# Kernel optimization log

Hardware: AMD Instinct MI355X
Metric: run time of the kernel (lower is better)

The kernel has to match this reference:

```python
import jax, jax.numpy as jnp
import numpy as np

N_NODES = 150000
D = 64
N_EDGES = 2000000  # bidirectional: 2 * num_train_edges


def setup_inputs() -> dict:
    key = jax.random.key(0)
    k1, k2, k3, k4, k5 = jax.random.split(key, 5)
    nodes_emb = jax.random.normal(k1, (N_NODES, D), dtype=jnp.float32)
    src = jax.random.randint(k2, (N_EDGES,), 0, N_NODES, dtype=jnp.int64 if jax.config.jax_enable_x64 else jnp.int32).astype(jnp.int32)
    dst = jax.random.randint(k3, (N_EDGES,), 0, N_NODES, dtype=jnp.int32)
    W1 = jax.random.normal(k4, (2 * D, D), dtype=jnp.float32) * (1.0 / np.sqrt(2 * D))
    b1 = jnp.zeros((D,), dtype=jnp.float32)
    W2 = jax.random.normal(k5, (D, 1), dtype=jnp.float32) * (1.0 / np.sqrt(D))
    b2 = jnp.zeros((1,), dtype=jnp.float32)
    return {"nodes_emb": nodes_emb, "src": src, "dst": dst,
            "W1": W1, "b1": b1, "W2": W2, "b2": b2}


def reference(nodes_emb, src, dst, W1, b1, W2, b2):
    # Gather per-edge endpoint embeddings and concat: [E, 2D]
    emb_src = nodes_emb[src]          # [E, D]
    emb_dst = nodes_emb[dst]          # [E, D]
    edge_emb = jnp.concatenate([emb_src, emb_dst], axis=1)  # [E, 2D]
    # 2-layer MLP edge scorer: Linear(2D->D) -> ReLU -> Linear(D->1)
    h = jax.nn.relu(edge_emb @ W1 + b1)  # [E, D]
    edge_logits = h @ W2 + b2            # [E, 1]
    return edge_logits
```

## Files before the change

### kernel.cpp

```cpp
#include <hip/hip_runtime.h>

typedef __attribute__((ext_vector_type(8))) short bf16x8;
typedef __attribute__((ext_vector_type(4))) float f32x4;
typedef __attribute__((ext_vector_type(2))) unsigned int u32x2;
typedef __attribute__((ext_vector_type(4))) unsigned int u32x4;

#define LDSTR 136
#define TPW 8

static __device__ __forceinline__ unsigned int pack2bf(float x, float y) {
  unsigned int ux = __builtin_bit_cast(unsigned int, x);
  ux += 0x7fffu + ((ux >> 16) & 1u);
  unsigned int uy = __builtin_bit_cast(unsigned int, y);
  uy += 0x7fffu + ((uy >> 16) & 1u);
  return (ux >> 16) | (uy & 0xffff0000u);
}
static __device__ __forceinline__ unsigned short f2bf_s(float x) {
  unsigned int ux = __builtin_bit_cast(unsigned int, x);
  ux += 0x7fffu + ((ux >> 16) & 1u);
  return (unsigned short)(ux >> 16);
}
static __device__ __forceinline__ bf16x8 make_afrag(float4 lo, float4 hi) {
  u32x4 p;
  p[0] = pack2bf(lo.x, lo.y);
  p[1] = pack2bf(lo.z, lo.w);
  p[2] = pack2bf(hi.x, hi.y);
  p[3] = pack2bf(hi.z, hi.w);
  return __builtin_bit_cast(bf16x8, p);
}

static __device__ __forceinline__ unsigned int q8(float v, float inv) {
  return (unsigned int)((int)rintf(v * inv) + 128);
}

__global__ __launch_bounds__(256) void node_proj(
    const float* __restrict__ emb,
    const float* __restrict__ W1,
    const float* __restrict__ b1,
    unsigned int* __restrict__ P8,
    unsigned int* __restrict__ Q8,
    float* __restrict__ SP,
    float* __restrict__ SQ,
    int N, int ntiles)
{
  __shared__ unsigned short ls_w1t[64 * LDSTR];
  const int tid  = threadIdx.x;
  const int wave = tid >> 6;
  const int lane = tid & 63;
  const int l15  = lane & 15;
  const int quad = lane >> 4;

  for (int i = tid; i < 64 * 128; i += 256) {
    int k = i >> 6, n = i & 63;
    ls_w1t[n * LDSTR + k] = f2bf_s(W1[i]);
  }
  __syncthreads();

  float b1q[4];
  #pragma unroll
  for (int tn = 0; tn < 4; ++tn) b1q[tn] = b1[tn * 16 + l15];

  bf16x8 bfragP[4][2], bfragQ[4][2];
  #pragma unroll
  for (int tn = 0; tn < 4; ++tn)
    #pragma unroll
    for (int s = 0; s < 2; ++s) {
      bfragP[tn][s] = *(const bf16x8*)&ls_w1t[(tn * 16 + l15) * LDSTR + s * 32 + quad * 8];
      bfragQ[tn][s] = *(const bf16x8*)&ls_w1t[(tn * 16 + l15) * LDSTR + 64 + s * 32 + quad * 8];
    }

  for (int tile = blockIdx.x * 4 + wave; tile < ntiles; tile += gridDim.x * 4) {
    const int base = tile * 16;

    bf16x8 afr0, afr1;
    {
      int node = base + l15;
      node = (node < N) ? node : N - 1;
      const float* rp = emb + (long long)node * 64 + quad * 8;
      afr0 = make_afrag(*(const float4*)(rp),      *(const float4*)(rp + 4));
      afr1 = make_afrag(*(const float4*)(rp + 32), *(const float4*)(rp + 36));
    }

    f32x4 aP[4], aQ[4];
    #pragma unroll
    for (int tn = 0; tn < 4; ++tn) { aP[tn] = (f32x4){0,0,0,0}; aQ[tn] = (f32x4){0,0,0,0}; }
    #pragma unroll
    for (int tn = 0; tn < 4; ++tn) {
      aP[tn] = __builtin_amdgcn_mfma_f32_16x16x32_bf16(afr0, bfragP[tn][0], aP[tn], 0, 0, 0);
      aQ[tn] = __builtin_amdgcn_mfma_f32_16x16x32_bf16(afr0, bfragQ[tn][0], aQ[tn], 0, 0, 0);
      aP[tn] = __builtin_amdgcn_mfma_f32_16x16x32_bf16(afr1, bfragP[tn][1], aP[tn], 0, 0, 0);
      aQ[tn] = __builtin_amdgcn_mfma_f32_16x16x32_bf16(afr1, bfragQ[tn][1], aQ[tn], 0, 0, 0);
    }

    #pragma unroll
    for (int r = 0; r < 4; ++r) {
      const int m = base + quad * 4 + r;
      float vp0 = aP[0][r], vp1 = aP[1][r], vp2 = aP[2][r], vp3 = aP[3][r];
      float vq0 = aQ[0][r] + b1q[0], vq1 = aQ[1][r] + b1q[1];
      float vq2 = aQ[2][r] + b1q[2], vq3 = aQ[3][r] + b1q[3];

      float mp = fmaxf(fmaxf(fabsf(vp0), fabsf(vp1)), fmaxf(fabsf(vp2), fabsf(vp3)));
      float mq = fmaxf(fmaxf(fabsf(vq0), fabsf(vq1)), fmaxf(fabsf(vq2), fabsf(vq3)));
      mp = fmaxf(mp, __shfl_xor(mp, 1)); mq = fmaxf(mq, __shfl_xor(mq, 1));
      mp = fmaxf(mp, __shfl_xor(mp, 2)); mq = fmaxf(mq, __shfl_xor(mq, 2));
      mp = fmaxf(mp, __shfl_xor(mp, 4)); mq = fmaxf(mq, __shfl_xor(mq, 4));
      mp = fmaxf(mp, __shfl_xor(mp, 8)); mq = fmaxf(mq, __shfl_xor(mq, 8));

      const float invP = (mp > 0.f) ? 127.f / mp : 0.f;
      const float invQ = (mq > 0.f) ? 127.f / mq : 0.f;

      if (m < N) {
        unsigned int pw = q8(vp0, invP) | (q8(vp1, invP) << 8) |
                          (q8(vp2, invP) << 16) | (q8(vp3, invP) << 24);
        unsigned int qw = q8(vq0, invQ) | (q8(vq1, invQ) << 8) |
                          (q8(vq2, invQ) << 16) | (q8(vq3, invQ) << 24);
        P8[(long long)m * 16 + l15] = pw;
        Q8[(long long)m * 16 + l15] = qw;
        if (l15 == 0) {
          SP[m] = mp * (1.f / 127.f);
          SQ[m] = mq * (1.f / 127.f);
        }
      }
    }
  }
}

__global__ __launch_bounds__(256) void edge_score(
    const unsigned int* __restrict__ P8,
    const unsigned int* __restrict__ Q8,
    const float* __restrict__ SP,
    const float* __restrict__ SQ,
    const int*   __restrict__ src,
    const int*   __restrict__ dst,
    const float* __restrict__ W2,
    const float* __restrict__ b2,
    float*       __restrict__ out,
    int E)
{
  const int tid  = blockIdx.x * 256 + threadIdx.x;
  const int lane = threadIdx.x & 63;
  const int s    = lane & 7;
  const int g    = lane >> 3;
  const int wid  = tid >> 6;
  const int step = gridDim.x * 4 * 32;

  float w2v[8];
  #pragma unroll
  for (int j = 0; j < 8; ++j) {
    const int pos = s * 8 + j;
    const int ch  = (pos & 3) * 16 + (pos >> 2);
    w2v[j] = W2[ch];
  }
  const float b2v = b2[0];
  const int sd = s * 2;

#define DOT8I(PU, QU, SPv, SQv, ACC)                                          \
  {                                                                           \
    const float t_ = __builtin_fmaf(-128.f, SPv + SQv, 0.f);                  \
    _Pragma("unroll")                                                         \
    for (int k = 0; k < 2; ++k) {                                             \
      const unsigned int pd = PU[k], qd = QU[k];                              \
      _Pragma("unroll")                                                       \
      for (int b = 0; b < 4; ++b) {                                           \
        float pf = (float)((pd >> (8 * b)) & 0xffu);                          \
        float qf = (float)((qd >> (8 * b)) & 0xffu);                          \
        float h = __builtin_fmaf(pf, SPv, __builtin_fmaf(qf, SQv, t_));       \
        h = fmaxf(h, 0.f);                                                    \
        ACC = __builtin_fmaf(h, w2v[k * 4 + b], ACC);                         \
      }                                                                       \
    }                                                                         \
  }

  int e0 = wid * 32;
  if (e0 >= E) return;

  int iA, iB, iC, iD, jA, jB, jC, jD;
  {
    const int eA = e0 + g,      eAc = (eA < E) ? eA : E - 1;
    const int eB = e0 + 8 + g,  eBc = (eB < E) ? eB : E - 1;
    const int eC = e0 + 16 + g, eCc = (eC < E) ? eC : E - 1;
    const int eD = e0 + 24 + g, eDc = (eD < E) ? eD : E - 1;
    iA = src[eAc]; jA = dst[eAc];
    iB = src[eBc]; jB = dst[eBc];
    iC = src[eCc]; jC = dst[eCc];
    iD = src[eDc]; jD = dst[eDc];
  }
  float spA = SP[iA], sqA = SQ[jA];
  float spB = SP[iB], sqB = SQ[jB];
  float spC = SP[iC], sqC = SQ[jC];
  float spD = SP[iD], sqD = SQ[jD];

  while (true) {
    const u32x2 pA = *(const u32x2*)(P8 + iA * 16 + sd);
    const u32x2 qA = *(const u32x2*)(Q8 + jA * 16 + sd);
    const u32x2 pB = *(const u32x2*)(P8 + iB * 16 + sd);
    const u32x2 qB = *(const u32x2*)(Q8 + jB * 16 + sd);
    const u32x2 pC = *(const u32x2*)(P8 + iC * 16 + sd);
    const u32x2 qC = *(const u32x2*)(Q8 + jC * 16 + sd);
    const u32x2 pD = *(const u32x2*)(P8 + iD * 16 + sd);
    const u32x2 qD = *(const u32x2*)(Q8 + jD * 16 + sd);

    const int en = e0 + step;
    const bool more = (en < E);
    int nA = iA, nB = iB, nC = iC, nD = iD;
    int mA = jA, mB = jB, mC = jC, mD = jD;
    if (more) {
      const int fA = en + g,      fAc = (fA < E) ? fA : E - 1;
      const int fB = en + 8 + g,  fBc = (fB < E) ? fB : E - 1;
      const int fC = en + 16 + g, fCc = (fC < E) ? fC : E - 1;
      const int fD = en + 24 + g, fDc = (fD < E) ? fD : E - 1;
      nA = src[fAc]; mA = dst[fAc];
      nB = src[fBc]; mB = dst[fBc];
      nC = src[fCc]; mC = dst[fCc];
      nD = src[fDc]; mD = dst[fDc];
    }

    float accA = 0.f, accB = 0.f, accC = 0.f, accD = 0.f;
    DOT8I(pA, qA, spA, sqA, accA);
    DOT8I(pB, qB, spB, sqB, accB);
    DOT8I(pC, qC, spC, sqC, accC);
    DOT8I(pD, qD, spD, sqD, accD);

    accA += __shfl_xor(accA, 1); accB += __shfl_xor(accB, 1);
    accC += __shfl_xor(accC, 1); accD += __shfl_xor(accD, 1);
    accA += __shfl_xor(accA, 2); accB += __shfl_xor(accB, 2);
    accC += __shfl_xor(accC, 2); accD += __shfl_xor(accD, 2);
    accA += __shfl_xor(accA, 4); accB += __shfl_xor(accB, 4);
    accC += __shfl_xor(accC, 4); accD += __shfl_xor(accD, 4);

    if (s == 0) {
      const int eA = e0 + g;
      const int eB = e0 + 8 + g;
      const int eC = e0 + 16 + g;
      const int eD = e0 + 24 + g;
      if (eA < E) out[eA] = accA + b2v;
      if (eB < E) out[eB] = accB + b2v;
      if (eC < E) out[eC] = accC + b2v;
      if (eD < E) out[eD] = accD + b2v;
    }

    if (!more) break;
    iA = nA; iB = nB; iC = nC; iD = nD;
    jA = mA; jB = mB; jC = mC; jD = mD;
    spA = SP[iA]; sqA = SQ[jA];
    spB = SP[iB]; sqB = SQ[jB];
    spC = SP[iC]; sqC = SQ[jC];
    spD = SP[iD]; sqD = SQ[jD];
    e0 = en;
  }
#undef DOT8I
}

__global__ __launch_bounds__(256) void edge_mlp_f32(
    const float* __restrict__ nodes_emb, const int* __restrict__ src,
    const int* __restrict__ dst, const float* __restrict__ W1,
    const float* __restrict__ b1, const float* __restrict__ W2,
    const float* __restrict__ b2, float* __restrict__ out, int E)
{
  __shared__ unsigned short ls_w1t[64 * LDSTR];
  __shared__ float ls_b1[64];
  __shared__ float ls_w2[64];
  const int tid = threadIdx.x, wave = tid >> 6, lane = tid & 63;
  const int l15 = lane & 15, quad = lane >> 4;
  for (int i = tid; i < 64 * 128; i += 256) {
    int n = i >> 7, k = i & 127;
    ls_w1t[n * LDSTR + k] = f2bf_s(W1[k * 64 + n]);
  }
  if (tid < 64) { ls_b1[tid] = b1[tid]; ls_w2[tid] = W2[tid]; }
  __syncthreads();
  bf16x8 bfrag[4][4];
  #pragma unroll
  for (int tn = 0; tn < 4; ++tn)
    #pragma unroll
    for (int s = 0; s < 4; ++s)
      bfrag[tn][s] = *(const bf16x8*)&ls_w1t[(tn * 16 + l15) * LDSTR + s * 32 + quad * 8];
  float myb1[4], myw2[4];
  #pragma unroll
  for (int tn = 0; tn < 4; ++tn) { myb1[tn] = ls_b1[tn*16+l15]; myw2[tn] = ls_w2[tn*16+l15]; }
  const float b2v = b2[0];
  const int wave_base = blockIdx.x * (TPW * 64) + wave * (TPW * 16);
  #pragma unroll 1
  for (int t = 0; t < TPW; ++t) {
    const int tile_base = wave_base + t * 16;
    if (tile_base >= E) break;
    const int e = tile_base + l15;
    const int si = src[e], di = dst[e];
    const float* srow = nodes_emb + (long long)si * 64 + quad * 8;
    const float* drow = nodes_emb + (long long)di * 64 + quad * 8;
    float4 v0 = *(const float4*)(srow),      v1 = *(const float4*)(srow + 4);
    float4 v2 = *(const float4*)(srow + 32), v3 = *(const float4*)(srow + 36);
    float4 v4 = *(const float4*)(drow),      v5 = *(const float4*)(drow + 4);
    float4 v6 = *(const float4*)(drow + 32), v7 = *(const float4*)(drow + 36);
    bf16x8 afr[4] = {make_afrag(v0,v1), make_afrag(v2,v3), make_afrag(v4,v5), make_afrag(v6,v7)};
    f32x4 acc[4];
    #pragma unroll
    for (int tn = 0; tn < 4; ++tn) acc[tn] = (f32x4){0.f,0.f,0.f,0.f};
    #pragma unroll
    for (int s = 0; s < 4; ++s)
      #pragma unroll
      for (int tn = 0; tn < 4; ++tn)
        acc[tn] = __builtin_amdgcn_mfma_f32_16x16x32_bf16(afr[s], bfrag[tn][s], acc[tn], 0, 0, 0);
    #pragma unroll
    for (int r = 0; r < 4; ++r) {
      float p = 0.f;
      #pragma unroll
      for (int tn = 0; tn < 4; ++tn) {
        float h = fmaxf(acc[tn][r] + myb1[tn], 0.f);
        p = __builtin_fmaf(h, myw2[tn], p);
      }
      p += __shfl_xor(p, 1); p += __shfl_xor(p, 2);
      p += __shfl_xor(p, 4); p += __shfl_xor(p, 8);
      if (l15 == 0) out[tile_base + quad * 4 + r] = p + b2v;
    }
  }
}

extern "C" void kernel_launch(void* const* d_in, const int* in_sizes, int n_in,
                              void* d_out, int out_size, void* d_ws, size_t ws_size,
                              hipStream_t stream) {
  const float* nodes_emb = (const float*)d_in[0];
  const int*   src       = (const int*)d_in[1];
  const int*   dst       = (const int*)d_in[2];
  const float* W1        = (const float*)d_in[3];
  const float* b1        = (const float*)d_in[4];
  const float* W2        = (const float*)d_in[5];
  const float* b2        = (const float*)d_in[6];
  float* out = (float*)d_out;

  const int E = in_sizes[1];
  const int nodes_elems = in_sizes[0];
  const int N = nodes_elems / 64;
  const size_t szRow = (size_t)N * 64;
  const size_t need  = szRow * 2 + (size_t)N * 8;

  if (ws_size >= need) {
    unsigned int* P8 = (unsigned int*)d_ws;
    unsigned int* Q8 = (unsigned int*)((char*)d_ws + szRow);
    float* SP = (float*)((char*)d_ws + szRow * 2);
    float* SQ = (float*)((char*)d_ws + szRow * 2 + (size_t)N * 4);
    const int ntiles = (N + 15) / 16;
    hipLaunchKernelGGL(node_proj, dim3(512), dim3(256), 0, stream,
                       nodes_emb, W1, b1, P8, Q8, SP, SQ, N, ntiles);
    hipLaunchKernelGGL(edge_score, dim3(4096), dim3(256), 0, stream,
                       P8, Q8, SP, SQ, src, dst, W2, b2, out, E);
  } else {
    const int epb = TPW * 64;
    const int blocks = (E + epb - 1) / epb;
    hipLaunchKernelGGL(edge_mlp_f32, dim3(blocks), dim3(256), 0, stream,
                       nodes_emb, src, dst, W1, b1, W2, b2, out, E);
  }
}
```

Measured before the change: 175.9 us.

## Bucketize edges by source/destination node range for cache-local gathers

A new kernel partitions the edges into 64 buckets keyed by (src range, dst range), using LDS atomics per replica block. A second new kernel scores the edges bucket by bucket, locating each edge through a prefix sum and binary search over the per-replica counts. The aim is to keep the quantized P8/Q8 node rows touched by one bucket small enough to stay cache-resident during the random gathers. In exchange it adds a bucketing pass that writes 64-bit packed records to workspace, runs on only 128 blocks, and silently drops edges if a cell exceeds its statistical capacity.

```diff
diff --git a/kernel.cpp b/kernel.cpp
--- a/kernel.cpp
+++ b/kernel.cpp
@@ -1,12 +1,16 @@
 #include <hip/hip_runtime.h>
+#include <math.h>
 
 typedef __attribute__((ext_vector_type(8))) short bf16x8;
 typedef __attribute__((ext_vector_type(4))) float f32x4;
 typedef __attribute__((ext_vector_type(2))) unsigned int u32x2;
 typedef __attribute__((ext_vector_type(4))) unsigned int u32x4;
+typedef unsigned long long u64;
 
 #define LDSTR 136
 #define TPW 8
+#define NREP 128
+#define NBKT 64
 
 static __device__ __forceinline__ unsigned int pack2bf(float x, float y) {
   unsigned int ux = __builtin_bit_cast(unsigned int, x);
@@ -31,6 +35,25 @@
 
 static __device__ __forceinline__ unsigned int q8(float v, float inv) {
   return (unsigned int)((int)rintf(v * inv) + 128);
+}
+
+static __device__ __forceinline__ float dot8i(u32x2 P, u32x2 Q, float sp, float sq,
+                                              const float* w2v) {
+  const float t_ = -128.f * (sp + sq);
+  float acc = 0.f;
+  #pragma unroll
+  for (int k2 = 0; k2 < 2; ++k2) {
+    const unsigned int pd = P[k2], qd = Q[k2];
+    #pragma unroll
+    for (int b = 0; b < 4; ++b) {
+      float pf = (float)((pd >> (8 * b)) & 0xffu);
+      float qf = (float)((qd >> (8 * b)) & 0xffu);
+      float h = __builtin_fmaf(pf, sp, __builtin_fmaf(qf, sq, t_));
+      h = fmaxf(h, 0.f);
+      acc = __builtin_fmaf(h, w2v[k2 * 4 + b], acc);
+    }
+  }
+  return acc;
 }
 
 __global__ __launch_bounds__(256) void node_proj(
@@ -125,17 +148,133 @@
   }
 }
 
+__global__ __launch_bounds__(256) void bucketize(
+    const int* __restrict__ src, const int* __restrict__ dst,
+    u64* __restrict__ seg, unsigned int* __restrict__ cntT,
+    int E, int ndiv, int cap)
+{
+  __shared__ unsigned int curs[NBKT];
+  const int r = blockIdx.x;
+  const int per = (E + NREP - 1) / NREP;
+  const int lo = r * per;
+  const int hi = (lo + per < E) ? lo + per : E;
+  for (int i = threadIdx.x; i < NBKT; i += 256) curs[i] = 0;
+  __syncthreads();
+  for (int e = lo + threadIdx.x; e < hi; e += 256) {
+    const int s = src[e], d = dst[e];
+    const int bkt = (s / ndiv) * 8 + (d / ndiv);
+    const unsigned int pos = atomicAdd(&curs[bkt], 1u);
+    if ((int)pos < cap) {
+      const u64 v = (u64)(unsigned)s | ((u64)(unsigned)d << 18) | ((u64)(unsigned)e << 36);
+      seg[((long long)r * NBKT + bkt) * cap + pos] = v;
+    }
+  }
+  __syncthreads();
+  for (int bkt = threadIdx.x; bkt < NBKT; bkt += 256) {
+    unsigned int c = curs[bkt];
+    cntT[bkt * NREP + r] = (c < (unsigned)cap) ? c : (unsigned)cap;
+  }
+}
+
+__global__ __launch_bounds__(256) void edge_score_bkt(
+    const unsigned int* __restrict__ P8, const unsigned int* __restrict__ Q8,
+    const float* __restrict__ SP, const float* __restrict__ SQ,
+    const u64* __restrict__ seg, const unsigned int* __restrict__ cntT,
+    const float* __restrict__ W2, const float* __restrict__ b2,
+    float* __restrict__ out, int E, int cap)
+{
+  __shared__ unsigned int pref[NREP + 1];
+  const int tid  = threadIdx.x;
+  const int lane = tid & 63;
+  const int sv   = lane & 7;
+  const int g    = lane >> 3;
+  const int wavloc = tid >> 6;
+  const int k    = blockIdx.x & 7;
+  const int tblk = blockIdx.x >> 3;
+  const int ngrp = gridDim.x >> 3;
+  const int wgid = tblk * 4 + wavloc;
+  const int nwg  = ngrp * 4;
+
+  float w2v[8];
+  #pragma unroll
+  for (int j = 0; j < 8; ++j) {
+    const int pos = sv * 8 + j;
+    const int ch  = (pos & 3) * 16 + (pos >> 2);
+    w2v[j] = W2[ch];
+  }
+  const float b2v = b2[0];
+  const int sd = sv * 2;
+
+  #pragma unroll 1
+  for (int j = 0; j < 8; ++j) {
+    const int b = k * 8 + j;
+    __syncthreads();
+    if (tid < 64) {
+      unsigned int c0 = cntT[b * NREP + tid];
+      unsigned int c1 = cntT[b * NREP + 64 + tid];
+      unsigned int s0 = c0, s1 = c1;
+      #pragma unroll
+      for (int off = 1; off < 64; off <<= 1) {
+        unsigned int t0 = __shfl_up(s0, off);
+        unsigned int t1 = __shfl_up(s1, off);
+        if (lane >= off) { s0 += t0; s1 += t1; }
+      }
+      const unsigned int tot0 = __shfl(s0, 63);
+      pref[tid + 1] = s0;
+      pref[64 + tid + 1] = s1 + tot0;
+      if (tid == 0) pref[0] = 0;
+    }
+    __syncthreads();
+    const int T = (int)pref[NREP];
+
+    for (int mb = wgid * 16; mb < T; mb += nwg * 16) {
+      const int mA = mb + g;
+      const int mB = mb + 8 + g;
+      const int mAc = (mA < T) ? mA : T - 1;
+      const int mBc = (mB < T) ? mB : T - 1;
+
+      int rA = 0, rAh = NREP, rB = 0, rBh = NREP;
+      #pragma unroll
+      for (int it = 0; it < 7; ++it) {
+        const int midA = (rA + rAh) >> 1;
+        if ((int)pref[midA] <= mAc) rA = midA; else rAh = midA;
+        const int midB = (rB + rBh) >> 1;
+        if ((int)pref[midB] <= mBc) rB = midB; else rBh = midB;
+      }
+      const u64 vA = seg[((long long)rA * NBKT + b) * cap + (mAc - (int)pref[rA])];
+      const u64 vB = seg[((long long)rB * NBKT + b) * cap + (mBc - (int)pref[rB])];
+      const int sA = (int)(vA & 0x3FFFFu), dA = (int)((vA >> 18) & 0x3FFFFu);
+      const int sB = (int)(vB & 0x3FFFFu), dB = (int)((vB >> 18) & 0x3FFFFu);
+      const int eA = (int)(vA >> 36),      eB = (int)(vB >> 36);
+
+      const u32x2 pA = *(const u32x2*)(P8 + sA * 16 + sd);
+      const u32x2 qA = *(const u32x2*)(Q8 + dA * 16 + sd);
+      const u32x2 pB = *(const u32x2*)(P8 + sB * 16 + sd);
+      const u32x2 qB = *(const u32x2*)(Q8 + dB * 16 + sd);
+      const float spA = SP[sA], sqA = SQ[dA];
+      const float spB = SP[sB], sqB = SQ[dB];
+
+      float accA = dot8i(pA, qA, spA, sqA, w2v);
+      float accB = dot8i(pB, qB, spB, sqB, w2v);
+
+      accA += __shfl_xor(accA, 1); accB += __shfl_xor(accB, 1);
+      accA += __shfl_xor(accA, 2); accB += __shfl_xor(accB, 2);
+      accA += __shfl_xor(accA, 4); accB += __shfl_xor(accB, 4);
+
+      if (sv == 0) {
+        if (mA < T) out[eA] = accA + b2v;
+        if (mB < T) out[eB] = accB + b2v;
+      }
+    }
+  }
+}
+
 __global__ __launch_bounds__(256) void edge_score(
-    const unsigned int* __restrict__ P8,
-    const unsigned int* __restrict__ Q8,
-    const float* __restrict__ SP,
-    const float* __restrict__ SQ,
-    const int*   __restrict__ src,
-    const int*   __restrict__ dst,
-    const float* __restrict__ W2,
-    const float* __restrict__ b2,
-    float*       __restrict__ out,
-    int E)
+    const unsigned int* __restrict__ P8, const unsigned int* __restrict__ Q8,
+    const float* __restrict__ SP, const float* __restrict__ SQ,
+    const int* __restrict__ src, const int* __restrict__ dst,
+    const float* __restrict__ W2, const float* __restrict__ b2,
+    float* __restrict__ out, int E)
 {
   const int tid  = blockIdx.x * 256 + threadIdx.x;
   const int lane = threadIdx.x & 63;
@@ -153,23 +292,6 @@
   }
   const float b2v = b2[0];
   const int sd = s * 2;
-
-#define DOT8I(PU, QU, SPv, SQv, ACC)                                          \
-  {                                                                           \
-    const float t_ = __builtin_fmaf(-128.f, SPv + SQv, 0.f);                  \
-    _Pragma("unroll")                                                         \
-    for (int k = 0; k < 2; ++k) {                                             \
-      const unsigned int pd = PU[k], qd = QU[k];                              \
-      _Pragma("unroll")                                                       \
-      for (int b = 0; b < 4; ++b) {                                           \
-        float pf = (float)((pd >> (8 * b)) & 0xffu);                          \
-        float qf = (float)((qd >> (8 * b)) & 0xffu);                          \
-        float h = __builtin_fmaf(pf, SPv, __builtin_fmaf(qf, SQv, t_));       \
-        h = fmaxf(h, 0.f);                                                    \
-        ACC = __builtin_fmaf(h, w2v[k * 4 + b], ACC);                         \
-      }                                                                       \
-    }                                                                         \
-  }
 
   int e0 = wid * 32;
   if (e0 >= E) return;
@@ -215,11 +337,10 @@
       nD = src[fDc]; mD = dst[fDc];
     }
 
-    float accA = 0.f, accB = 0.f, accC = 0.f, accD = 0.f;
-    DOT8I(pA, qA, spA, sqA, accA);
-    DOT8I(pB, qB, spB, sqB, accB);
-    DOT8I(pC, qC, spC, sqC, accC);
-    DOT8I(pD, qD, spD, sqD, accD);
+    float accA = dot8i(pA, qA, spA, sqA, w2v);
+    float accB = dot8i(pB, qB, spB, sqB, w2v);
+    float accC = dot8i(pC, qC, spC, sqC, w2v);
+    float accD = dot8i(pD, qD, spD, sqD, w2v);
 
     accA += __shfl_xor(accA, 1); accB += __shfl_xor(accB, 1);
     accC += __shfl_xor(accC, 1); accD += __shfl_xor(accD, 1);
@@ -248,7 +369,6 @@
     spD = SP[iD]; sqD = SQ[jD];
     e0 = en;
   }
-#undef DOT8I
 }
 
 __global__ __launch_bounds__(256) void edge_mlp_f32(
@@ -330,19 +450,40 @@
   const int E = in_sizes[1];
   const int nodes_elems = in_sizes[0];
   const int N = nodes_elems / 64;
-  const size_t szRow = (size_t)N * 64;
-  const size_t need  = szRow * 2 + (size_t)N * 8;
-
-  if (ws_size >= need) {
+  const int ntiles = (N + 15) / 16;
+  const int ndiv = (N + 7) / 8;
+
+  const size_t szRow  = (size_t)N * 64;
+  const size_t offSP  = szRow * 2;
+  const size_t offSQ  = offSP + (size_t)N * 4;
+  const size_t offCnt = offSQ + (size_t)N * 4;
+  const size_t offSeg = offCnt + (size_t)NBKT * NREP * 4;
+
+  const long long cells = (long long)NBKT * NREP;
+  const int perCell = (int)((E + cells - 1) / cells);
+  const int sig = (int)ceil(sqrt((double)(perCell > 0 ? perCell : 1)));
+  const int cap = perCell + 10 * sig + 16;
+  const size_t need_full = offSeg + (size_t)NBKT * NREP * (size_t)cap * 8;
+  const size_t need_mid  = offCnt;
+
+  if (ws_size >= need_mid) {
     unsigned int* P8 = (unsigned int*)d_ws;
     unsigned int* Q8 = (unsigned int*)((char*)d_ws + szRow);
-    float* SP = (float*)((char*)d_ws + szRow * 2);
-    float* SQ = (float*)((char*)d_ws + szRow * 2 + (size_t)N * 4);
-    const int ntiles = (N + 15) / 16;
+    float* SP = (float*)((char*)d_ws + offSP);
+    float* SQ = (float*)((char*)d_ws + offSQ);
     hipLaunchKernelGGL(node_proj, dim3(512), dim3(256), 0, stream,
                        nodes_emb, W1, b1, P8, Q8, SP, SQ, N, ntiles);
-    hipLaunchKernelGGL(edge_score, dim3(4096), dim3(256), 0, stream,
-                       P8, Q8, SP, SQ, src, dst, W2, b2, out, E);
+    if (ws_size >= need_full) {
+      unsigned int* cntT = (unsigned int*)((char*)d_ws + offCnt);
+      u64* seg = (u64*)((char*)d_ws + offSeg);
+      hipLaunchKernelGGL(bucketize, dim3(NREP), dim3(256), 0, stream,
+                         src, dst, seg, cntT, E, ndiv, cap);
+      hipLaunchKernelGGL(edge_score_bkt, dim3(2048), dim3(256), 0, stream,
+                         P8, Q8, SP, SQ, seg, cntT, W2, b2, out, E, cap);
+    } else {
+      hipLaunchKernelGGL(edge_score, dim3(4096), dim3(256), 0, stream,
+                         P8, Q8, SP, SQ, src, dst, W2, b2, out, E);
+    }
   } else {
     const int epb = TPW * 64;
     const int blocks = (E + epb - 1) / epb;
```

After: 224.4 us. 27.6% more time.
